# Kernel tuning notes

Measured on AMD Instinct MI355X. Metric: run time of the kernel, lower is better.

The kernel has to match this reference:

```python
import jax, jax.numpy as jnp
import numpy as np

B, S, D = 2, 2048, 768
NH, GH = 12, 4
HD = D // NH            # 64
GD = HD * GH            # 256 (grouped KV projection width)
REP = NH // GH          # 3  (repeat factor for KV heads)
SCALE = HD ** -0.5
MASK_FILL = -1e-09      # faithful to the original (NOT -1e9)


def setup_inputs() -> dict:
    key = jax.random.key(0)
    ks = jax.random.split(key, 9)
    init = 0.02
    x = jax.random.normal(ks[0], (B, S, D), dtype=jnp.float32)
    masks = jnp.tril(jnp.ones((S, S), dtype=jnp.float32)) > 0  # bool causal mask
    Wq = jax.random.normal(ks[1], (D, D), dtype=jnp.float32) * init
    bq = jnp.zeros((D,), dtype=jnp.float32)
    Wk = jax.random.normal(ks[2], (D, GD), dtype=jnp.float32) * init
    bk = jnp.zeros((GD,), dtype=jnp.float32)
    Wv = jax.random.normal(ks[3], (D, GD), dtype=jnp.float32) * init
    bv = jnp.zeros((GD,), dtype=jnp.float32)
    Wo = jax.random.normal(ks[4], (D, D), dtype=jnp.float32) * init
    bo = jnp.zeros((D,), dtype=jnp.float32)
    return {"x": x, "masks": masks, "Wq": Wq, "bq": bq, "Wk": Wk, "bk": bk,
            "Wv": Wv, "bv": bv, "Wo": Wo, "bo": bo}


def reference(x, masks, Wq, bq, Wk, bk, Wv, bv, Wo, bo):
    bs, seq, _ = x.shape
    # projections (weights stored [in, out])
    q = (x @ Wq + bq).reshape(bs, seq, NH, HD).transpose(0, 2, 1, 3)   # [b, nh, s, hd]
    k = (x @ Wk + bk).reshape(bs, seq, GH, HD).transpose(0, 2, 1, 3)   # [b, gh, s, hd]
    v = (x @ Wv + bv).reshape(bs, seq, GH, HD).transpose(0, 2, 1, 3)
    # repeat_interleave KV heads to match query heads (faithful to original)
    k = jnp.repeat(k, REP, axis=1)                                     # [b, nh, s, hd]
    v = jnp.repeat(v, REP, axis=1)
    scores = jnp.einsum('bhqd,bhkd->bhqk', q, k) * SCALE               # [b, nh, s, s]
    # original: masked_fill(masks == 0, -1e-09)
    scores = jnp.where(masks, scores, MASK_FILL)
    attn = jax.nn.softmax(scores, axis=-1)
    out = jnp.einsum('bhqk,bhkd->bhqd', attn, v)                       # [b, nh, s, hd]
    # faithful to original buggy merge: transpose(-1,-2).contiguous().view(b, s, dim)
    out = out.transpose(0, 1, 3, 2).reshape(bs, seq, D)
    return out @ Wo + bo
```

## Files before the change

### kernel.cpp

```cpp
#include <hip/hip_runtime.h>
#include <stdint.h>


typedef unsigned short ushort_t;
typedef short bf16x8 __attribute__((ext_vector_type(8)));
typedef float f32x4 __attribute__((ext_vector_type(4)));

#define MFMA(a, b, c) __builtin_amdgcn_mfma_f32_16x16x32_bf16((a), (b), (c), 0, 0, 0)

__device__ __forceinline__ ushort_t f2bf(float f) {
    union { float f; unsigned u; } v; v.f = f;
    const unsigned r = v.u + 0x7FFFu + ((v.u >> 16) & 1u);
    return (ushort_t)(r >> 16);
}

__global__ __launch_bounds__(256) void prep_x(const float* __restrict__ x,
                                              ushort_t* __restrict__ xb) {
    const int i = (blockIdx.x * 256 + threadIdx.x) * 4;
    const float4 v = *(const float4*)(x + i);
    uint2 p;
    p.x = (unsigned)f2bf(v.x) | ((unsigned)f2bf(v.y) << 16);
    p.y = (unsigned)f2bf(v.z) | ((unsigned)f2bf(v.w) << 16);
    *(uint2*)(xb + i) = p;
}

__global__ __launch_bounds__(256) void prep_w(
    const float* __restrict__ Wq, const float* __restrict__ Wk,
    const float* __restrict__ Wv, const float* __restrict__ Wo,
    ushort_t* __restrict__ WqT, ushort_t* __restrict__ WkT,
    ushort_t* __restrict__ WvT, ushort_t* __restrict__ WoT) {
    const int z = blockIdx.z;
    const float* src; ushort_t* dst; int N;
    if (z == 0)      { src = Wq; dst = WqT; N = 768; }
    else if (z == 1) { src = Wk; dst = WkT; N = 256; }
    else if (z == 2) { src = Wv; dst = WvT; N = 256; }
    else             { src = Wo; dst = WoT; N = 768; }
    const int k0 = blockIdx.x * 64, n0 = blockIdx.y * 64;
    if (n0 >= N) return;

    __shared__ float Ts[64][65];
    const int tid = threadIdx.x;
    const int r = tid >> 2, cb = (tid & 3) * 16;
    #pragma unroll
    for (int jj = 0; jj < 4; ++jj) {
        const float4 v = *(const float4*)(src + (k0 + r) * N + n0 + cb + jj * 4);
        Ts[cb + jj * 4 + 0][r] = v.x; Ts[cb + jj * 4 + 1][r] = v.y;
        Ts[cb + jj * 4 + 2][r] = v.z; Ts[cb + jj * 4 + 3][r] = v.w;
    }
    __syncthreads();
    const int n = tid >> 2, kc = (tid & 3) * 16;
    unsigned hbuf[16];
    #pragma unroll
    for (int j = 0; j < 16; ++j) hbuf[j] = f2bf(Ts[n][kc + j]);
    uint4 p0, p1;
    p0.x = hbuf[0] | (hbuf[1] << 16);   p0.y = hbuf[2] | (hbuf[3] << 16);
    p0.z = hbuf[4] | (hbuf[5] << 16);   p0.w = hbuf[6] | (hbuf[7] << 16);
    p1.x = hbuf[8] | (hbuf[9] << 16);   p1.y = hbuf[10] | (hbuf[11] << 16);
    p1.z = hbuf[12] | (hbuf[13] << 16); p1.w = hbuf[14] | (hbuf[15] << 16);
    *(uint4*)(dst + (n0 + n) * 768 + k0 + kc) = p0;
    *(uint4*)(dst + (n0 + n) * 768 + k0 + kc + 8) = p1;
}

__global__ __launch_bounds__(256) void qkv_kernel(
    const ushort_t* __restrict__ xb,
    const ushort_t* __restrict__ WqT, const ushort_t* __restrict__ WkT,
    const ushort_t* __restrict__ WvT,
    const float* __restrict__ bq, const float* __restrict__ bk,
    const float* __restrict__ bv,
    ushort_t* __restrict__ Qb, ushort_t* __restrict__ Kb,
    ushort_t* __restrict__ Vtb) {
    const int ct = blockIdx.x, rt = blockIdx.y;
    const int r0 = rt * 64;
    const ushort_t* WT; const float* bias; int head; int kind;
    if (ct < 12)      { WT = WqT; bias = bq; head = ct;      kind = 0; }
    else if (ct < 16) { WT = WkT; bias = bk; head = ct - 12; kind = 1; }
    else              { WT = WvT; bias = bv; head = ct - 16; kind = 2; }
    const int n0 = head * 64;

    __shared__ uint4 Xs[512];
    __shared__ uint4 Ws[512];

    const int tid = threadIdx.x;
    const int lane = tid & 63, w = tid >> 6;
    const int quad = lane >> 4, l15 = lane & 15;
    const int sr = tid >> 2, sb = (tid & 3) * 2;

    f32x4 acc[4] = {{0,0,0,0},{0,0,0,0},{0,0,0,0},{0,0,0,0}};

    for (int k0 = 0; k0 < 768; k0 += 64) {
        __syncthreads();
        #pragma unroll
        for (int c = 0; c < 2; ++c) {
            const int blk = sb + c;
            Xs[sr * 8 + (blk ^ (sr & 7))] = *(const uint4*)(xb + (r0 + sr) * 768 + k0 + blk * 8);
            Ws[sr * 8 + (blk ^ (sr & 7))] = *(const uint4*)(WT + (n0 + sr) * 768 + k0 + blk * 8);
        }
        __syncthreads();
        #pragma unroll
        for (int ks = 0; ks < 2; ++ks) {
            const int arow = 16 * w + l15;
            const bf16x8 af = *(const bf16x8*)&Xs[arow * 8 + ((quad + 4 * ks) ^ (arow & 7))];
            #pragma unroll
            for (int ctt = 0; ctt < 4; ++ctt) {
                const int brow = 16 * ctt + l15;
                const bf16x8 bfr = *(const bf16x8*)&Ws[brow * 8 + ((quad + 4 * ks) ^ (brow & 7))];
                acc[ctt] = MFMA(af, bfr, acc[ctt]);
            }
        }
    }
    #pragma unroll
    for (int ctt = 0; ctt < 4; ++ctt) {
        const int cd = ctt * 16 + l15;
        const float bv_ = bias[n0 + cd];
        const int row0 = r0 + 16 * w + quad * 4;
        const int b = row0 >> 11;
        if (kind == 2) {
            const int s0 = row0 & 2047;
            unsigned h[4];
            #pragma unroll
            for (int reg = 0; reg < 4; ++reg) h[reg] = f2bf(acc[ctt][reg] + bv_);
            uint2 pk; pk.x = h[0] | (h[1] << 16); pk.y = h[2] | (h[3] << 16);
            *(uint2*)(Vtb + ((b * 4 + head) * 64 + cd) * 2048 + s0) = pk;
        } else {
            #pragma unroll
            for (int reg = 0; reg < 4; ++reg) {
                const int row = row0 + reg;
                const int s = row & 2047;
                const ushort_t h = f2bf(acc[ctt][reg] + bv_);
                if (kind == 0) Qb[((b * 12 + head) * 2048 + s) * 64 + cd] = h;
                else           Kb[((b * 4 + head) * 2048 + s) * 64 + cd] = h;
            }
        }
    }
}

__global__ __launch_bounds__(256) void attn_kernel(
    const ushort_t* __restrict__ Qb, const ushort_t* __restrict__ Kb,
    const ushort_t* __restrict__ Vtb,
    ushort_t* __restrict__ aT_hi, ushort_t* __restrict__ aT_lo) {
    const int qt = blockIdx.x, h = blockIdx.y, b = blockIdx.z;
    const int g = h / 3;
    const int q0 = qt * 64;
    const int tid = threadIdx.x;
    const int lane = tid & 63, w = tid >> 6;
    const int quad = lane >> 4, l15 = lane & 15;

    __shared__ uint4 K_l[512];
    __shared__ uint4 V_l[512];
    __shared__ __align__(16) ushort_t P_l[64 * 72];

    const ushort_t* Qp = Qb + ((b * 12 + h) * 2048 + q0 + 16 * w + l15) * 64;
    const bf16x8 qf0 = *(const bf16x8*)(Qp + quad * 8);
    const bf16x8 qf1 = *(const bf16x8*)(Qp + 32 + quad * 8);

    const ushort_t* Kp = Kb + (b * 4 + g) * 2048 * 64;
    const ushort_t* Vp = Vtb + (b * 4 + g) * 64 * 2048;

    f32x4 o[4] = {{0,0,0,0},{0,0,0,0},{0,0,0,0},{0,0,0,0}};
    float lacc[4] = {0.f, 0.f, 0.f, 0.f};

    const int sr = tid >> 2, sb = (tid & 3) * 2;
    const int qg = q0 + 16 * w + quad * 4;

    for (int k0 = 0; k0 < 2048; k0 += 64) {
        __syncthreads();
        #pragma unroll
        for (int c = 0; c < 2; ++c) {
            const int blk = sb + c;
            K_l[sr * 8 + (blk ^ (sr & 7))] = *(const uint4*)(Kp + (k0 + sr) * 64 + blk * 8);
            V_l[sr * 8 + (blk ^ (sr & 7))] = *(const uint4*)(Vp + sr * 2048 + k0 + blk * 8);
        }
        __syncthreads();
        #pragma unroll
        for (int ctt = 0; ctt < 4; ++ctt) {
            const int key = ctt * 16 + l15;
            f32x4 s = {0, 0, 0, 0};
            s = MFMA(qf0, *(const bf16x8*)&K_l[key * 8 + ((quad + 0) ^ (key & 7))], s);
            s = MFMA(qf1, *(const bf16x8*)&K_l[key * 8 + ((quad + 4) ^ (key & 7))], s);
            const int kg = k0 + key;
            #pragma unroll
            for (int reg = 0; reg < 4; ++reg) {
                const float sv = (kg <= qg + reg) ? s[reg] * 0.125f : -1e-9f;
                const float e = __expf(sv);
                lacc[reg] += e;
                P_l[(16 * w + quad * 4 + reg) * 72 + key] = f2bf(e);
            }
        }
        const bf16x8 pf0 = *(const bf16x8*)&P_l[(16 * w + l15) * 72 + quad * 8];
        const bf16x8 pf1 = *(const bf16x8*)&P_l[(16 * w + l15) * 72 + 32 + quad * 8];
        #pragma unroll
        for (int ctt = 0; ctt < 4; ++ctt) {
            const int d = ctt * 16 + l15;
            o[ctt] = MFMA(pf0, *(const bf16x8*)&V_l[d * 8 + ((quad + 0) ^ (d & 7))], o[ctt]);
            o[ctt] = MFMA(pf1, *(const bf16x8*)&V_l[d * 8 + ((quad + 4) ^ (d & 7))], o[ctt]);
        }
    }
    #pragma unroll
    for (int reg = 0; reg < 4; ++reg) {
        float v = lacc[reg];
        v += __shfl_xor(v, 1); v += __shfl_xor(v, 2);
        v += __shfl_xor(v, 4); v += __shfl_xor(v, 8);
        lacc[reg] = 1.f / v;
    }
    const int t0 = q0 + 16 * w + quad * 4;
    #pragma unroll
    for (int ctt = 0; ctt < 4; ++ctt) {
        const int d = ctt * 16 + l15;
        unsigned hh[4], hl[4];
        #pragma unroll
        for (int reg = 0; reg < 4; ++reg) {
            const float val = o[ctt][reg] * lacc[reg];
            const ushort_t hi = f2bf(val);
            union { unsigned u; float f; } vv; vv.u = (unsigned)hi << 16;
            hh[reg] = hi;
            hl[reg] = f2bf(val - vv.f);
        }
        const int idx = (b * 768 + h * 64 + d) * 2048 + t0;
        uint2 ph, pl;
        ph.x = hh[0] | (hh[1] << 16); ph.y = hh[2] | (hh[3] << 16);
        pl.x = hl[0] | (hl[1] << 16); pl.y = hl[2] | (hl[3] << 16);
        *(uint2*)(aT_hi + idx) = ph;
        *(uint2*)(aT_lo + idx) = pl;
    }
}

__global__ __launch_bounds__(256) void out_proj_kernel(
    const ushort_t* __restrict__ aT_hi, const ushort_t* __restrict__ aT_lo,
    const ushort_t* __restrict__ WoT, const float* __restrict__ bo,
    float* __restrict__ out) {
    const int ct = blockIdx.x, rt = blockIdx.y;
    const int r0 = rt * 64, c0 = ct * 64;
    __shared__ uint4 Ah[512];
    __shared__ uint4 Al[512];
    __shared__ uint4 Ws[512];
    const int tid = threadIdx.x;
    const int lane = tid & 63, w = tid >> 6;
    const int quad = lane >> 4, l15 = lane & 15;
    const int sr = tid >> 2, sb = (tid & 3) * 2;

    f32x4 acc[4] = {{0,0,0,0},{0,0,0,0},{0,0,0,0},{0,0,0,0}};

    for (int k0 = 0; k0 < 768; k0 += 64) {
        __syncthreads();
        #pragma unroll
        for (int c = 0; c < 2; ++c) {
            const int blk = sb + c;
            const int slot = sr * 8 + (blk ^ (sr & 7));
            Ah[slot] = *(const uint4*)(aT_hi + (r0 + sr) * 768 + k0 + blk * 8);
            Al[slot] = *(const uint4*)(aT_lo + (r0 + sr) * 768 + k0 + blk * 8);
            Ws[slot] = *(const uint4*)(WoT + (c0 + sr) * 768 + k0 + blk * 8);
        }
        __syncthreads();
        #pragma unroll
        for (int ks = 0; ks < 2; ++ks) {
            const int arow = 16 * w + l15;
            const int aslot = arow * 8 + ((quad + 4 * ks) ^ (arow & 7));
            const bf16x8 ah = *(const bf16x8*)&Ah[aslot];
            const bf16x8 al = *(const bf16x8*)&Al[aslot];
            #pragma unroll
            for (int ctt = 0; ctt < 4; ++ctt) {
                const int brow = 16 * ctt + l15;
                const bf16x8 bfr = *(const bf16x8*)&Ws[brow * 8 + ((quad + 4 * ks) ^ (brow & 7))];
                acc[ctt] = MFMA(ah, bfr, acc[ctt]);
                acc[ctt] = MFMA(al, bfr, acc[ctt]);
            }
        }
    }
    #pragma unroll
    for (int ctt = 0; ctt < 4; ++ctt) {
        const int cd = c0 + ctt * 16 + l15;
        const float bo_v = bo[cd];
        #pragma unroll
        for (int reg = 0; reg < 4; ++reg) {
            const int row = r0 + 16 * w + quad * 4 + reg;
            out[row * 768 + cd] = acc[ctt][reg] + bo_v;
        }
    }
}

extern "C" void kernel_launch(void* const* d_in, const int* in_sizes, int n_in,
                              void* d_out, int out_size, void* d_ws, size_t ws_size,
                              hipStream_t stream) {
    const float* x  = (const float*)d_in[0];
    const float* Wq = (const float*)d_in[2];
    const float* bq = (const float*)d_in[3];
    const float* Wk = (const float*)d_in[4];
    const float* bk = (const float*)d_in[5];
    const float* Wv = (const float*)d_in[6];
    const float* bv = (const float*)d_in[7];
    const float* Wo = (const float*)d_in[8];
    const float* bo = (const float*)d_in[9];
    float* out = (float*)d_out;

    uint8_t* wsb = (uint8_t*)d_ws;
    ushort_t* xb    = (ushort_t*)(wsb);
    ushort_t* WqT   = (ushort_t*)(wsb + 6291456);
    ushort_t* WkT   = (ushort_t*)(wsb + 7471104);
    ushort_t* WvT   = (ushort_t*)(wsb + 7864320);
    ushort_t* WoT   = (ushort_t*)(wsb + 8257536);
    ushort_t* Qb    = (ushort_t*)(wsb + 9437184);
    ushort_t* Kb    = (ushort_t*)(wsb + 15728640);
    ushort_t* Vtb   = (ushort_t*)(wsb + 17825792);
    ushort_t* aT_hi = (ushort_t*)(wsb + 19922944);
    ushort_t* aT_lo = (ushort_t*)(wsb + 26214400);

    prep_x<<<3072, 256, 0, stream>>>(x, xb);
    prep_w<<<dim3(12, 12, 4), 256, 0, stream>>>(Wq, Wk, Wv, Wo, WqT, WkT, WvT, WoT);
    qkv_kernel<<<dim3(20, 64), 256, 0, stream>>>(xb, WqT, WkT, WvT, bq, bk, bv, Qb, Kb, Vtb);
    attn_kernel<<<dim3(32, 12, 2), 256, 0, stream>>>(Qb, Kb, Vtb, aT_hi, aT_lo);
    out_proj_kernel<<<dim3(12, 64), 256, 0, stream>>>(aT_hi, aT_lo, WoT, bo, out);
}
```

Before: 204.0 us.

## Skip fully masked key tiles via V suffix sums, enlarge GEMM row tiles

Masked scores are filled with -1e-9, so their exp is effectively 1. The attention kernel now stops at the diagonal tile and adds the precomputed suffix sum of V for the remaining keys, plus a constant count to the softmax denominator. This roughly halves attention work, at the cost of a new small suffix-sum kernel and a reliance on exp(-1e-9) being treated as exactly 1. The QKV and output-projection GEMMs now use 128-row tiles for more reuse of the weight tiles. Query tiles are launched in reverse order so the longest ones start first, and P values are written as packed bf16 pairs.

```diff
diff --git a/kernel.cpp b/kernel.cpp
--- a/kernel.cpp
+++ b/kernel.cpp
@@ -1,4 +1,5 @@
 #include <hip/hip_runtime.h>
+#include <hip/hip_bf16.h>
 #include <stdint.h>
 
 
@@ -12,6 +13,16 @@
     union { float f; unsigned u; } v; v.f = f;
     const unsigned r = v.u + 0x7FFFu + ((v.u >> 16) & 1u);
     return (ushort_t)(r >> 16);
+}
+__device__ __forceinline__ unsigned pk2(float a, float b) {
+    __hip_bfloat162 h = __float22bfloat162_rn(make_float2(a, b));
+    unsigned u; __builtin_memcpy(&u, &h, 4); return u;
+}
+__device__ __forceinline__ float bflo(unsigned u) {
+    union { unsigned u; float f; } v; v.u = u << 16; return v.f;
+}
+__device__ __forceinline__ float bfhi(unsigned u) {
+    union { unsigned u; float f; } v; v.u = u & 0xFFFF0000u; return v.f;
 }
 
 __global__ __launch_bounds__(256) void prep_x(const float* __restrict__ x,
@@ -70,76 +81,115 @@
     ushort_t* __restrict__ Qb, ushort_t* __restrict__ Kb,
     ushort_t* __restrict__ Vtb) {
     const int ct = blockIdx.x, rt = blockIdx.y;
-    const int r0 = rt * 64;
+    const int r0 = rt * 128;
     const ushort_t* WT; const float* bias; int head; int kind;
     if (ct < 12)      { WT = WqT; bias = bq; head = ct;      kind = 0; }
     else if (ct < 16) { WT = WkT; bias = bk; head = ct - 12; kind = 1; }
     else              { WT = WvT; bias = bv; head = ct - 16; kind = 2; }
     const int n0 = head * 64;
 
-    __shared__ uint4 Xs[512];
+    __shared__ uint4 Xs[1024];
     __shared__ uint4 Ws[512];
 
     const int tid = threadIdx.x;
     const int lane = tid & 63, w = tid >> 6;
     const int quad = lane >> 4, l15 = lane & 15;
-    const int sr = tid >> 2, sb = (tid & 3) * 2;
-
-    f32x4 acc[4] = {{0,0,0,0},{0,0,0,0},{0,0,0,0},{0,0,0,0}};
+    const int srX = tid >> 1, sbX = (tid & 1) * 4;
+    const int srW = tid >> 2, sbW = (tid & 3) * 2;
+
+    f32x4 acc[2][4] = {};
 
     for (int k0 = 0; k0 < 768; k0 += 64) {
         __syncthreads();
         #pragma unroll
+        for (int c = 0; c < 4; ++c) {
+            const int blk = sbX + c;
+            Xs[srX * 8 + (blk ^ (srX & 7))] = *(const uint4*)(xb + (r0 + srX) * 768 + k0 + blk * 8);
+        }
+        #pragma unroll
         for (int c = 0; c < 2; ++c) {
-            const int blk = sb + c;
-            Xs[sr * 8 + (blk ^ (sr & 7))] = *(const uint4*)(xb + (r0 + sr) * 768 + k0 + blk * 8);
-            Ws[sr * 8 + (blk ^ (sr & 7))] = *(const uint4*)(WT + (n0 + sr) * 768 + k0 + blk * 8);
+            const int blk = sbW + c;
+            Ws[srW * 8 + (blk ^ (srW & 7))] = *(const uint4*)(WT + (n0 + srW) * 768 + k0 + blk * 8);
         }
         __syncthreads();
         #pragma unroll
         for (int ks = 0; ks < 2; ++ks) {
-            const int arow = 16 * w + l15;
-            const bf16x8 af = *(const bf16x8*)&Xs[arow * 8 + ((quad + 4 * ks) ^ (arow & 7))];
+            const int a0r = 32 * w + l15, a1r = 32 * w + 16 + l15;
+            const bf16x8 af0 = *(const bf16x8*)&Xs[a0r * 8 + ((quad + 4 * ks) ^ (a0r & 7))];
+            const bf16x8 af1 = *(const bf16x8*)&Xs[a1r * 8 + ((quad + 4 * ks) ^ (a1r & 7))];
             #pragma unroll
             for (int ctt = 0; ctt < 4; ++ctt) {
                 const int brow = 16 * ctt + l15;
                 const bf16x8 bfr = *(const bf16x8*)&Ws[brow * 8 + ((quad + 4 * ks) ^ (brow & 7))];
-                acc[ctt] = MFMA(af, bfr, acc[ctt]);
-            }
-        }
-    }
-    #pragma unroll
-    for (int ctt = 0; ctt < 4; ++ctt) {
-        const int cd = ctt * 16 + l15;
-        const float bv_ = bias[n0 + cd];
-        const int row0 = r0 + 16 * w + quad * 4;
-        const int b = row0 >> 11;
-        if (kind == 2) {
-            const int s0 = row0 & 2047;
-            unsigned h[4];
-            #pragma unroll
-            for (int reg = 0; reg < 4; ++reg) h[reg] = f2bf(acc[ctt][reg] + bv_);
-            uint2 pk; pk.x = h[0] | (h[1] << 16); pk.y = h[2] | (h[3] << 16);
-            *(uint2*)(Vtb + ((b * 4 + head) * 64 + cd) * 2048 + s0) = pk;
-        } else {
-            #pragma unroll
-            for (int reg = 0; reg < 4; ++reg) {
-                const int row = row0 + reg;
-                const int s = row & 2047;
-                const ushort_t h = f2bf(acc[ctt][reg] + bv_);
-                if (kind == 0) Qb[((b * 12 + head) * 2048 + s) * 64 + cd] = h;
-                else           Kb[((b * 4 + head) * 2048 + s) * 64 + cd] = h;
-            }
+                acc[0][ctt] = MFMA(af0, bfr, acc[0][ctt]);
+                acc[1][ctt] = MFMA(af1, bfr, acc[1][ctt]);
+            }
+        }
+    }
+    #pragma unroll
+    for (int half = 0; half < 2; ++half) {
+        #pragma unroll
+        for (int ctt = 0; ctt < 4; ++ctt) {
+            const int cd = ctt * 16 + l15;
+            const float bv_ = bias[n0 + cd];
+            const int row0 = r0 + 32 * w + 16 * half + quad * 4;
+            const int b = row0 >> 11;
+            if (kind == 2) {
+                const int s0 = row0 & 2047;
+                unsigned h[4];
+                #pragma unroll
+                for (int reg = 0; reg < 4; ++reg) h[reg] = f2bf(acc[half][ctt][reg] + bv_);
+                uint2 pkv; pkv.x = h[0] | (h[1] << 16); pkv.y = h[2] | (h[3] << 16);
+                *(uint2*)(Vtb + ((b * 4 + head) * 64 + cd) * 2048 + s0) = pkv;
+            } else {
+                #pragma unroll
+                for (int reg = 0; reg < 4; ++reg) {
+                    const int row = row0 + reg;
+                    const int s = row & 2047;
+                    const ushort_t h = f2bf(acc[half][ctt][reg] + bv_);
+                    if (kind == 0) Qb[((b * 12 + head) * 2048 + s) * 64 + cd] = h;
+                    else           Kb[((b * 4 + head) * 2048 + s) * 64 + cd] = h;
+                }
+            }
+        }
+    }
+}
+
+__global__ __launch_bounds__(256) void vsuffix_kernel(
+    const ushort_t* __restrict__ Vtb, float* __restrict__ Vsuf) {
+    const int bg = blockIdx.x;
+    const int tid = threadIdx.x;
+    const int d = tid & 63, part = tid >> 6;
+    __shared__ float ts[32][64];
+    const ushort_t* base = Vtb + (bg * 64 + d) * 2048;
+    for (int t = part * 8; t < part * 8 + 8; ++t) {
+        float sum = 0.f;
+        #pragma unroll
+        for (int j8 = 0; j8 < 8; ++j8) {
+            const uint4 v = *(const uint4*)(base + t * 64 + j8 * 8);
+            sum += bflo(v.x) + bfhi(v.x) + bflo(v.y) + bfhi(v.y)
+                 + bflo(v.z) + bfhi(v.z) + bflo(v.w) + bfhi(v.w);
+        }
+        ts[t][d] = sum;
+    }
+    __syncthreads();
+    if (tid < 64) {
+        float acc = 0.f;
+        Vsuf[(bg * 33 + 32) * 64 + tid] = 0.f;
+        for (int t = 31; t >= 0; --t) {
+            acc += ts[t][tid];
+            Vsuf[(bg * 33 + t) * 64 + tid] = acc;
         }
     }
 }
 
 __global__ __launch_bounds__(256) void attn_kernel(
     const ushort_t* __restrict__ Qb, const ushort_t* __restrict__ Kb,
-    const ushort_t* __restrict__ Vtb,
+    const ushort_t* __restrict__ Vtb, const float* __restrict__ Vsuf,
     ushort_t* __restrict__ aT_hi, ushort_t* __restrict__ aT_lo) {
-    const int qt = blockIdx.x, h = blockIdx.y, b = blockIdx.z;
+    const int qt = 31 - blockIdx.x, h = blockIdx.y, b = blockIdx.z;
     const int g = h / 3;
+    const int bg = b * 4 + g;
     const int q0 = qt * 64;
     const int tid = threadIdx.x;
     const int lane = tid & 63, w = tid >> 6;
@@ -153,16 +203,17 @@
     const bf16x8 qf0 = *(const bf16x8*)(Qp + quad * 8);
     const bf16x8 qf1 = *(const bf16x8*)(Qp + 32 + quad * 8);
 
-    const ushort_t* Kp = Kb + (b * 4 + g) * 2048 * 64;
-    const ushort_t* Vp = Vtb + (b * 4 + g) * 64 * 2048;
+    const ushort_t* Kp = Kb + bg * 2048 * 64;
+    const ushort_t* Vp = Vtb + bg * 64 * 2048;
 
     f32x4 o[4] = {{0,0,0,0},{0,0,0,0},{0,0,0,0},{0,0,0,0}};
-    float lacc[4] = {0.f, 0.f, 0.f, 0.f};
+    float lsum = 0.f;
 
     const int sr = tid >> 2, sb = (tid & 3) * 2;
-    const int qg = q0 + 16 * w + quad * 4;
-
-    for (int k0 = 0; k0 < 2048; k0 += 64) {
+    const int thr = 16 * w + l15;
+    ushort_t* Prow = P_l + (16 * w + l15) * 72;
+
+    for (int k0 = 0; k0 <= q0; k0 += 64) {
         __syncthreads();
         #pragma unroll
         for (int c = 0; c < 2; ++c) {
@@ -171,19 +222,36 @@
             V_l[sr * 8 + (blk ^ (sr & 7))] = *(const uint4*)(Vp + sr * 2048 + k0 + blk * 8);
         }
         __syncthreads();
-        #pragma unroll
-        for (int ctt = 0; ctt < 4; ++ctt) {
-            const int key = ctt * 16 + l15;
-            f32x4 s = {0, 0, 0, 0};
-            s = MFMA(qf0, *(const bf16x8*)&K_l[key * 8 + ((quad + 0) ^ (key & 7))], s);
-            s = MFMA(qf1, *(const bf16x8*)&K_l[key * 8 + ((quad + 4) ^ (key & 7))], s);
-            const int kg = k0 + key;
-            #pragma unroll
-            for (int reg = 0; reg < 4; ++reg) {
-                const float sv = (kg <= qg + reg) ? s[reg] * 0.125f : -1e-9f;
-                const float e = __expf(sv);
-                lacc[reg] += e;
-                P_l[(16 * w + quad * 4 + reg) * 72 + key] = f2bf(e);
+        if (k0 < q0) {
+            #pragma unroll
+            for (int ctt = 0; ctt < 4; ++ctt) {
+                const int key = ctt * 16 + l15;
+                f32x4 s = {0, 0, 0, 0};
+                s = MFMA(*(const bf16x8*)&K_l[key * 8 + ((quad + 0) ^ (key & 7))], qf0, s);
+                s = MFMA(*(const bf16x8*)&K_l[key * 8 + ((quad + 4) ^ (key & 7))], qf1, s);
+                const float e0 = __expf(s[0] * 0.125f), e1 = __expf(s[1] * 0.125f);
+                const float e2 = __expf(s[2] * 0.125f), e3 = __expf(s[3] * 0.125f);
+                lsum += (e0 + e1) + (e2 + e3);
+                uint2 pw; pw.x = pk2(e0, e1); pw.y = pk2(e2, e3);
+                *(uint2*)(Prow + ctt * 16 + quad * 4) = pw;
+            }
+        } else {
+            #pragma unroll
+            for (int ctt = 0; ctt < 4; ++ctt) {
+                const int key = ctt * 16 + l15;
+                f32x4 s = {0, 0, 0, 0};
+                s = MFMA(*(const bf16x8*)&K_l[key * 8 + ((quad + 0) ^ (key & 7))], qf0, s);
+                s = MFMA(*(const bf16x8*)&K_l[key * 8 + ((quad + 4) ^ (key & 7))], qf1, s);
+                const int base = ctt * 16 + quad * 4;
+                float e[4];
+                #pragma unroll
+                for (int reg = 0; reg < 4; ++reg) {
+                    const float sv = (base + reg <= thr) ? s[reg] * 0.125f : -1e-9f;
+                    e[reg] = __expf(sv);
+                    lsum += e[reg];
+                }
+                uint2 pw; pw.x = pk2(e[0], e[1]); pw.y = pk2(e[2], e[3]);
+                *(uint2*)(Prow + ctt * 16 + quad * 4) = pw;
             }
         }
         const bf16x8 pf0 = *(const bf16x8*)&P_l[(16 * w + l15) * 72 + quad * 8];
@@ -195,21 +263,22 @@
             o[ctt] = MFMA(pf1, *(const bf16x8*)&V_l[d * 8 + ((quad + 4) ^ (d & 7))], o[ctt]);
         }
     }
-    #pragma unroll
-    for (int reg = 0; reg < 4; ++reg) {
-        float v = lacc[reg];
-        v += __shfl_xor(v, 1); v += __shfl_xor(v, 2);
-        v += __shfl_xor(v, 4); v += __shfl_xor(v, 8);
-        lacc[reg] = 1.f / v;
-    }
+    float ls = lsum;
+    ls += __shfl_xor(ls, 16); ls += __shfl_xor(ls, 32);
+    const float invv = 1.f / (ls + (float)(1984 - q0));
+    float inv_r[4];
+    #pragma unroll
+    for (int reg = 0; reg < 4; ++reg) inv_r[reg] = __shfl(invv, quad * 4 + reg);
+    const float* vsp = Vsuf + (bg * 33 + qt + 1) * 64;
     const int t0 = q0 + 16 * w + quad * 4;
     #pragma unroll
     for (int ctt = 0; ctt < 4; ++ctt) {
         const int d = ctt * 16 + l15;
+        const float vs = vsp[d];
         unsigned hh[4], hl[4];
         #pragma unroll
         for (int reg = 0; reg < 4; ++reg) {
-            const float val = o[ctt][reg] * lacc[reg];
+            const float val = (o[ctt][reg] + vs) * inv_r[reg];
             const ushort_t hi = f2bf(val);
             union { unsigned u; float f; } vv; vv.u = (unsigned)hi << 16;
             hh[reg] = hi;
@@ -229,51 +298,64 @@
     const ushort_t* __restrict__ WoT, const float* __restrict__ bo,
     float* __restrict__ out) {
     const int ct = blockIdx.x, rt = blockIdx.y;
-    const int r0 = rt * 64, c0 = ct * 64;
-    __shared__ uint4 Ah[512];
-    __shared__ uint4 Al[512];
+    const int r0 = rt * 128, c0 = ct * 64;
+    __shared__ uint4 Ah[1024];
+    __shared__ uint4 Al[1024];
     __shared__ uint4 Ws[512];
     const int tid = threadIdx.x;
     const int lane = tid & 63, w = tid >> 6;
     const int quad = lane >> 4, l15 = lane & 15;
-    const int sr = tid >> 2, sb = (tid & 3) * 2;
-
-    f32x4 acc[4] = {{0,0,0,0},{0,0,0,0},{0,0,0,0},{0,0,0,0}};
+    const int srX = tid >> 1, sbX = (tid & 1) * 4;
+    const int srW = tid >> 2, sbW = (tid & 3) * 2;
+
+    f32x4 acc[2][4] = {};
 
     for (int k0 = 0; k0 < 768; k0 += 64) {
         __syncthreads();
         #pragma unroll
+        for (int c = 0; c < 4; ++c) {
+            const int blk = sbX + c;
+            const int slot = srX * 8 + (blk ^ (srX & 7));
+            Ah[slot] = *(const uint4*)(aT_hi + (r0 + srX) * 768 + k0 + blk * 8);
+            Al[slot] = *(const uint4*)(aT_lo + (r0 + srX) * 768 + k0 + blk * 8);
+        }
+        #pragma unroll
         for (int c = 0; c < 2; ++c) {
-            const int blk = sb + c;
-            const int slot = sr * 8 + (blk ^ (sr & 7));
-            Ah[slot] = *(const uint4*)(aT_hi + (r0 + sr) * 768 + k0 + blk * 8);
-            Al[slot] = *(const uint4*)(aT_lo + (r0 + sr) * 768 + k0 + blk * 8);
-            Ws[slot] = *(const uint4*)(WoT + (c0 + sr) * 768 + k0 + blk * 8);
+            const int blk = sbW + c;
+            Ws[srW * 8 + (blk ^ (srW & 7))] = *(const uint4*)(WoT + (c0 + srW) * 768 + k0 + blk * 8);
         }
         __syncthreads();
         #pragma unroll
         for (int ks = 0; ks < 2; ++ks) {
-            const int arow = 16 * w + l15;
-            const int aslot = arow * 8 + ((quad + 4 * ks) ^ (arow & 7));
-            const bf16x8 ah = *(const bf16x8*)&Ah[aslot];
-            const bf16x8 al = *(const bf16x8*)&Al[aslot];
+            const int a0r = 32 * w + l15, a1r = 32 * w + 16 + l15;
+            const int s0 = a0r * 8 + ((quad + 4 * ks) ^ (a0r & 7));
+            const int s1 = a1r * 8 + ((quad + 4 * ks) ^ (a1r & 7));
+            const bf16x8 ah0 = *(const bf16x8*)&Ah[s0];
+            const bf16x8 ah1 = *(const bf16x8*)&Ah[s1];
+            const bf16x8 al0 = *(const bf16x8*)&Al[s0];
+            const bf16x8 al1 = *(const bf16x8*)&Al[s1];
             #pragma unroll
             for (int ctt = 0; ctt < 4; ++ctt) {
                 const int brow = 16 * ctt + l15;
                 const bf16x8 bfr = *(const bf16x8*)&Ws[brow * 8 + ((quad + 4 * ks) ^ (brow & 7))];
-                acc[ctt] = MFMA(ah, bfr, acc[ctt]);
-                acc[ctt] = MFMA(al, bfr, acc[ctt]);
-            }
-        }
-    }
-    #pragma unroll
-    for (int ctt = 0; ctt < 4; ++ctt) {
-        const int cd = c0 + ctt * 16 + l15;
-        const float bo_v = bo[cd];
-        #pragma unroll
-        for (int reg = 0; reg < 4; ++reg) {
-            const int row = r0 + 16 * w + quad * 4 + reg;
-            out[row * 768 + cd] = acc[ctt][reg] + bo_v;
+                acc[0][ctt] = MFMA(ah0, bfr, acc[0][ctt]);
+                acc[0][ctt] = MFMA(al0, bfr, acc[0][ctt]);
+                acc[1][ctt] = MFMA(ah1, bfr, acc[1][ctt]);
+                acc[1][ctt] = MFMA(al1, bfr, acc[1][ctt]);
+            }
+        }
+    }
+    #pragma unroll
+    for (int half = 0; half < 2; ++half) {
+        #pragma unroll
+        for (int ctt = 0; ctt < 4; ++ctt) {
+            const int cd = c0 + ctt * 16 + l15;
+            const float bo_v = bo[cd];
+            #pragma unroll
+            for (int reg = 0; reg < 4; ++reg) {
+                const int row = r0 + 32 * w + 16 * half + quad * 4 + reg;
+                out[row * 768 + cd] = acc[half][ctt][reg] + bo_v;
+            }
         }
     }
 }
@@ -301,12 +383,14 @@
     ushort_t* Qb    = (ushort_t*)(wsb + 9437184);
     ushort_t* Kb    = (ushort_t*)(wsb + 15728640);
     ushort_t* Vtb   = (ushort_t*)(wsb + 17825792);
-    ushort_t* aT_hi = (ushort_t*)(wsb + 19922944);
-    ushort_t* aT_lo = (ushort_t*)(wsb + 26214400);
+    float*    Vsuf  = (float*)   (wsb + 19922944);
+    ushort_t* aT_hi = (ushort_t*)(wsb + 19990528);
+    ushort_t* aT_lo = (ushort_t*)(wsb + 26281984);
 
     prep_x<<<3072, 256, 0, stream>>>(x, xb);
     prep_w<<<dim3(12, 12, 4), 256, 0, stream>>>(Wq, Wk, Wv, Wo, WqT, WkT, WvT, WoT);
-    qkv_kernel<<<dim3(20, 64), 256, 0, stream>>>(xb, WqT, WkT, WvT, bq, bk, bv, Qb, Kb, Vtb);
-    attn_kernel<<<dim3(32, 12, 2), 256, 0, stream>>>(Qb, Kb, Vtb, aT_hi, aT_lo);
-    out_proj_kernel<<<dim3(12, 64), 256, 0, stream>>>(aT_hi, aT_lo, WoT, bo, out);
-}
+    qkv_kernel<<<dim3(20, 32), 256, 0, stream>>>(xb, WqT, WkT, WvT, bq, bk, bv, Qb, Kb, Vtb);
+    vsuffix_kernel<<<8, 256, 0, stream>>>(Vtb, Vsuf);
+    attn_kernel<<<dim3(32, 12, 2), 256, 0, stream>>>(Qb, Kb, Vtb, Vsuf, aT_hi, aT_lo);
+    out_proj_kernel<<<dim3(12, 32), 256, 0, stream>>>(aT_hi, aT_lo, WoT, bo, out);
+}
```

Result: slower. 208.1 us (+2.0%).
